# Kernel tuning notes

Hardware: AMD Instinct MI355X
Metric: run time of the kernel (lower is better)

Reference implementation:

```python
import jax, jax.numpy as jnp
import numpy as np


def conv2d_relu(x, W, b, stride=1):
    # x: NHWC, W: HWIO
    y = jax.lax.conv_general_dilated(x, W, (stride, stride), 'VALID',
                                     dimension_numbers=('NHWC', 'HWIO', 'NHWC'))
    return jax.nn.relu(y + b)


def maxpool_3x3_s2(x):
    return jax.lax.reduce_window(x, -jnp.inf, jax.lax.max,
                                 (1, 3, 3, 1), (1, 2, 2, 1), 'VALID')


def locally_connected_relu(x, W, b, k, stride=1):
    # x: [B, H, W, C]; W: [oh, ow, C*k*k, F]; b: [oh, ow, F]
    # Extract patches -> [B, oh, ow, C*k*k], then per-position GEMM.
    p = jax.lax.conv_general_dilated_patches(
        x, (k, k), (stride, stride), 'VALID',
        dimension_numbers=('NHWC', 'HWIO', 'NHWC'))
    return jax.nn.relu(jnp.einsum('bijp,ijpf->bijf', p, W) + b)


def setup_inputs() -> dict:
    key = jax.random.key(0)
    ks = jax.random.split(key, 16)
    s = 0.02  # small init so relu/sigmoid stay in a sane range
    inp = {
        'inputs': jax.random.normal(ks[0], (32, 152, 152, 3), dtype=jnp.float32),
        'W1': jax.random.normal(ks[1], (11, 11, 3, 32), dtype=jnp.float32) * s,
        'b1': jnp.zeros((32,), jnp.float32),
        'W3': jax.random.normal(ks[2], (9, 9, 32, 16), dtype=jnp.float32) * s,
        'b3': jnp.zeros((16,), jnp.float32),
        'LW4': jax.random.normal(ks[3], (54, 54, 9 * 9 * 16, 16), dtype=jnp.float32) * s,
        'Lb4': jnp.zeros((54, 54, 16), jnp.float32),
        'LW5': jax.random.normal(ks[4], (24, 24, 7 * 7 * 16, 16), dtype=jnp.float32) * s,
        'Lb5': jnp.zeros((24, 24, 16), jnp.float32),
        'LW6': jax.random.normal(ks[5], (20, 20, 5 * 5 * 16, 16), dtype=jnp.float32) * s,
        'Lb6': jnp.zeros((20, 20, 16), jnp.float32),
        'W7': jax.random.normal(ks[6], (6400, 4096), dtype=jnp.float32) * s,
        'b7': jnp.zeros((4096,), jnp.float32),
        'W8': jax.random.normal(ks[7], (4096, 1), dtype=jnp.float32) * s,
        'b8': jnp.zeros((1,), jnp.float32),
    }
    return inp


def reference(inputs, W1, b1, W3, b3, LW4, Lb4, LW5, Lb5, LW6, Lb6, W7, b7, W8, b8):
    x = conv2d_relu(inputs, W1, b1)          # [B,142,142,32]
    x = maxpool_3x3_s2(x)                    # [B,70,70,32]
    x = conv2d_relu(x, W3, b3)               # [B,62,62,16]
    x = locally_connected_relu(x, LW4, Lb4, 9, 1)   # [B,54,54,16]
    x = locally_connected_relu(x, LW5, Lb5, 7, 2)   # [B,24,24,16]
    x = locally_connected_relu(x, LW6, Lb6, 5, 1)   # [B,20,20,16]
    x = x.reshape(x.shape[0], -1)            # [B,6400]
    x = jax.nn.relu(x @ W7 + b7)             # [B,4096]  (Dropout is identity at inference)
    return jax.nn.sigmoid(x @ W8 + b8)       # [B,1]
```

## Files before the change

### kernel.cpp

```cpp
#include <hip/hip_runtime.h>
#include <math.h>

#define DEV_INLINE __device__ __forceinline__

DEV_INLINE float relu_f(float v) { return v > 0.f ? v : 0.f; }

DEV_INLINE void fma4(float4& a, float s, const float4& v) {
    a.x += s * v.x; a.y += s * v.y; a.z += s * v.z; a.w += s * v.w;
}

__global__ __launch_bounds__(256, 2) void k_conv1(
    const float* __restrict__ x, const float* __restrict__ W,
    const float* __restrict__ b, float* __restrict__ y)
{
    __shared__ float sw[11 * 11 * 3 * 32];
    __shared__ float sx[26 * 42 * 3];
    const int n   = blockIdx.z;
    const int oh0 = blockIdx.y * 16;
    const int ow0 = blockIdx.x * 32;
    const int tid = threadIdx.x;

    for (int i = tid; i < 11616; i += 256) sw[i] = W[i];

    const float* xn = x + (size_t)n * 152 * 152 * 3;
    for (int i = tid; i < 26 * 42 * 3; i += 256) {
        int c = i % 3; int t = i / 3; int col = t % 42; int row = t / 42;
        int r  = oh0 + row; if (r > 151) r = 151;
        int cc = ow0 + col; if (cc > 151) cc = 151;
        sx[i] = xn[(r * 152 + cc) * 3 + c];
    }
    __syncthreads();

    const int ty = tid >> 4, tx = tid & 15;
    float acc[2][32];
#pragma unroll
    for (int p = 0; p < 2; ++p)
#pragma unroll
        for (int j = 0; j < 32; ++j) acc[p][j] = 0.f;

    for (int kh = 0; kh < 11; ++kh) {
        for (int kw = 0; kw < 11; ++kw) {
#pragma unroll
            for (int ic = 0; ic < 3; ++ic) {
                float x0 = sx[((ty + kh) * 42 + (tx + kw)) * 3 + ic];
                float x1 = sx[((ty + kh) * 42 + (tx + 16 + kw)) * 3 + ic];
                const float4* wp4 = (const float4*)&sw[((kh * 11 + kw) * 3 + ic) * 32];
#pragma unroll
                for (int j4 = 0; j4 < 8; ++j4) {
                    float4 w = wp4[j4];
                    acc[0][j4 * 4 + 0] += x0 * w.x;
                    acc[0][j4 * 4 + 1] += x0 * w.y;
                    acc[0][j4 * 4 + 2] += x0 * w.z;
                    acc[0][j4 * 4 + 3] += x0 * w.w;
                    acc[1][j4 * 4 + 0] += x1 * w.x;
                    acc[1][j4 * 4 + 1] += x1 * w.y;
                    acc[1][j4 * 4 + 2] += x1 * w.z;
                    acc[1][j4 * 4 + 3] += x1 * w.w;
                }
            }
        }
    }

#pragma unroll
    for (int p = 0; p < 2; ++p) {
        int oh = oh0 + ty, ow = ow0 + tx + p * 16;
        if (oh < 142 && ow < 142) {
            float* yp = y + (((size_t)n * 142 + oh) * 142 + ow) * 32;
#pragma unroll
            for (int j = 0; j < 32; ++j) yp[j] = relu_f(acc[p][j] + b[j]);
        }
    }
}

__global__ void k_pool(const float* __restrict__ x, float* __restrict__ y)
{
    int idx = blockIdx.x * 256 + threadIdx.x;
    if (idx >= 32 * 70 * 70 * 8) return;
    int c4 = idx & 7; int t = idx >> 3;
    int pw = t % 70; t /= 70; int ph = t % 70; int n = t / 70;
    const float* xp = x + (((size_t)n * 142 + ph * 2) * 142 + pw * 2) * 32 + c4 * 4;
    float4 m = make_float4(-1e30f, -1e30f, -1e30f, -1e30f);
#pragma unroll
    for (int r = 0; r < 3; ++r) {
#pragma unroll
        for (int cc = 0; cc < 3; ++cc) {
            float4 v = *(const float4*)(xp + ((size_t)r * 142 + cc) * 32);
            m.x = fmaxf(m.x, v.x); m.y = fmaxf(m.y, v.y);
            m.z = fmaxf(m.z, v.z); m.w = fmaxf(m.w, v.w);
        }
    }
    *(float4*)(y + (size_t)idx * 4) = m;
}

__global__ __launch_bounds__(128, 2) void k_conv3(
    const float* __restrict__ x, const float* __restrict__ W,
    const float* __restrict__ bias, float* __restrict__ y)
{
    __shared__ float sw[81 * 8 * 16];
    __shared__ float sx[16 * 40 * 8];
    const int n   = blockIdx.z;
    const int oh0 = blockIdx.y * 8;
    const int ow0 = blockIdx.x * 32;
    const int tid = threadIdx.x;
    const int ty = tid >> 4, tx = tid & 15;
    const float* xn = x + (size_t)n * 70 * 70 * 32;

    float acc[2][16];
#pragma unroll
    for (int p = 0; p < 2; ++p)
#pragma unroll
        for (int j = 0; j < 16; ++j) acc[p][j] = 0.f;

    for (int icc = 0; icc < 4; ++icc) {
        const int ic0 = icc * 8;
        __syncthreads();
        for (int i = tid; i < 10368; i += 128) {
            int oc = i & 15; int t = i >> 4; int ic = t & 7; int q = t >> 3;
            sw[i] = W[(q * 32 + ic0 + ic) * 16 + oc];
        }
        for (int i = tid; i < 5120; i += 128) {
            int ic = i & 7; int t = i >> 3; int col = t % 40; int row = t / 40;
            int r  = oh0 + row; if (r > 69) r = 69;
            int cc = ow0 + col; if (cc > 69) cc = 69;
            sx[i] = xn[(r * 70 + cc) * 32 + ic0 + ic];
        }
        __syncthreads();

        for (int kh = 0; kh < 9; ++kh) {
            for (int kw = 0; kw < 9; ++kw) {
                const int q = kh * 9 + kw;
#pragma unroll
                for (int ic = 0; ic < 8; ++ic) {
                    float x0 = sx[((ty + kh) * 40 + tx + kw) * 8 + ic];
                    float x1 = sx[((ty + kh) * 40 + tx + 16 + kw) * 8 + ic];
                    const float4* wp4 = (const float4*)&sw[(q * 8 + ic) * 16];
#pragma unroll
                    for (int j4 = 0; j4 < 4; ++j4) {
                        float4 w = wp4[j4];
                        acc[0][j4 * 4 + 0] += x0 * w.x;
                        acc[0][j4 * 4 + 1] += x0 * w.y;
                        acc[0][j4 * 4 + 2] += x0 * w.z;
                        acc[0][j4 * 4 + 3] += x0 * w.w;
                        acc[1][j4 * 4 + 0] += x1 * w.x;
                        acc[1][j4 * 4 + 1] += x1 * w.y;
                        acc[1][j4 * 4 + 2] += x1 * w.z;
                        acc[1][j4 * 4 + 3] += x1 * w.w;
                    }
                }
            }
        }
    }

#pragma unroll
    for (int p = 0; p < 2; ++p) {
        int oh = oh0 + ty, ow = ow0 + tx + p * 16;
        if (oh < 62 && ow < 62) {
            float* yp = y + (((size_t)n * 62 + oh) * 62 + ow) * 16;
#pragma unroll
            for (int j = 0; j < 16; ++j) yp[j] = relu_f(acc[p][j] + bias[j]);
        }
    }
}

template <int K, int S, int XD, int OD>
__global__ __launch_bounds__(64) void k_lc(
    const float* __restrict__ x, const float* __restrict__ W,
    const float* __restrict__ bias, float* __restrict__ y)
{
    constexpr int K2 = K * K;
    constexpr int P  = 16 * K2;
    __shared__ int soff[K2];
    const int i = blockIdx.y, j = blockIdx.x;
    const int tid = threadIdx.x;
    for (int t = tid; t < K2; t += 64) {
        int kh = t / K, kw = t % K;
        soff[t] = ((i * S + kh) * XD + (j * S + kw)) * 16;
    }
    __syncthreads();

    const int fq = tid & 3, b0 = tid >> 2;
    const float* xb0 = x + (size_t)b0 * XD * XD * 16;
    const float* xb1 = xb0 + (size_t)16 * XD * XD * 16;
    const float* wp  = W + ((size_t)(i * OD + j) * P) * 16 + fq * 4;

    float4 a0 = make_float4(0.f, 0.f, 0.f, 0.f);
    float4 a1 = make_float4(0.f, 0.f, 0.f, 0.f);

    for (int q = 0; q < K2; ++q) {
        const int ro = soff[q];
#pragma unroll
        for (int c4 = 0; c4 < 4; ++c4) {
            const float4 xv0 = *(const float4*)(xb0 + ro + c4 * 4);
            const float4 xv1 = *(const float4*)(xb1 + ro + c4 * 4);
            const float4 w0 = *(const float4*)(wp + ((c4 * 4 + 0) * K2 + q) * 16);
            const float4 w1 = *(const float4*)(wp + ((c4 * 4 + 1) * K2 + q) * 16);
            const float4 w2 = *(const float4*)(wp + ((c4 * 4 + 2) * K2 + q) * 16);
            const float4 w3 = *(const float4*)(wp + ((c4 * 4 + 3) * K2 + q) * 16);
            fma4(a0, xv0.x, w0); fma4(a0, xv0.y, w1); fma4(a0, xv0.z, w2); fma4(a0, xv0.w, w3);
            fma4(a1, xv1.x, w0); fma4(a1, xv1.y, w1); fma4(a1, xv1.z, w2); fma4(a1, xv1.w, w3);
        }
    }

    const float4 bv = *(const float4*)(bias + ((size_t)i * OD + j) * 16 + fq * 4);
    a0.x = relu_f(a0.x + bv.x); a0.y = relu_f(a0.y + bv.y);
    a0.z = relu_f(a0.z + bv.z); a0.w = relu_f(a0.w + bv.w);
    a1.x = relu_f(a1.x + bv.x); a1.y = relu_f(a1.y + bv.y);
    a1.z = relu_f(a1.z + bv.z); a1.w = relu_f(a1.w + bv.w);
    *(float4*)(y + (((size_t)b0 * OD + i) * OD + j) * 16 + fq * 4) = a0;
    *(float4*)(y + (((size_t)(b0 + 16) * OD + i) * OD + j) * 16 + fq * 4) = a1;
}

__global__ __launch_bounds__(256) void k_fc7(
    const float* __restrict__ x, const float* __restrict__ W,
    float* __restrict__ part)
{
    const int o  = blockIdx.x * 256 + threadIdx.x;
    const int k0 = blockIdx.y * 400;
    float acc[32];
#pragma unroll
    for (int b = 0; b < 32; ++b) acc[b] = 0.f;
    const float* wp = W + (size_t)k0 * 4096 + o;
    for (int kk = 0; kk < 400; kk += 2) {
        float w0 = wp[(size_t)kk * 4096];
        float w1 = wp[(size_t)(kk + 1) * 4096];
#pragma unroll
        for (int b = 0; b < 32; ++b) {
            float2 xv = *(const float2*)(x + (size_t)b * 6400 + k0 + kk);
            acc[b] += xv.x * w0 + xv.y * w1;
        }
    }
    float* pp = part + ((size_t)blockIdx.y * 32) * 4096 + o;
#pragma unroll
    for (int b = 0; b < 32; ++b) pp[(size_t)b * 4096] = acc[b];
}

__global__ __launch_bounds__(256) void k_fc8(
    const float* __restrict__ part, const float* __restrict__ b7,
    const float* __restrict__ W8, const float* __restrict__ b8,
    float* __restrict__ out)
{
    const int b = blockIdx.x, tid = threadIdx.x;
    float s = 0.f;
    for (int o = tid; o < 4096; o += 256) {
        float v = b7[o];
#pragma unroll
        for (int kb = 0; kb < 16; ++kb) v += part[((size_t)kb * 32 + b) * 4096 + o];
        v = relu_f(v);
        s += v * W8[o];
    }
#pragma unroll
    for (int off = 32; off > 0; off >>= 1) s += __shfl_down(s, off, 64);
    __shared__ float red[4];
    if ((tid & 63) == 0) red[tid >> 6] = s;
    __syncthreads();
    if (tid == 0) {
        float t = red[0] + red[1] + red[2] + red[3] + b8[0];
        out[b] = 1.f / (1.f + expf(-t));
    }
}

extern "C" void kernel_launch(void* const* d_in, const int* in_sizes, int n_in,
                              void* d_out, int out_size, void* d_ws, size_t ws_size,
                              hipStream_t stream)
{
    (void)in_sizes; (void)n_in; (void)out_size; (void)ws_size;
    const float* x   = (const float*)d_in[0];
    const float* W1  = (const float*)d_in[1];
    const float* b1  = (const float*)d_in[2];
    const float* W3  = (const float*)d_in[3];
    const float* b3  = (const float*)d_in[4];
    const float* LW4 = (const float*)d_in[5];
    const float* Lb4 = (const float*)d_in[6];
    const float* LW5 = (const float*)d_in[7];
    const float* Lb5 = (const float*)d_in[8];
    const float* LW6 = (const float*)d_in[9];
    const float* Lb6 = (const float*)d_in[10];
    const float* W7  = (const float*)d_in[11];
    const float* b7  = (const float*)d_in[12];
    const float* W8  = (const float*)d_in[13];
    const float* b8  = (const float*)d_in[14];
    float* out = (float*)d_out;

    float* ws = (float*)d_ws;
    float* y1 = ws;
    float* y2 = ws + 20647936;
    float* y3 = ws;
    float* y4 = ws + 1968128;
    float* y5 = ws + 3461120;
    float* y6 = ws + 3756032;
    float* p7 = ws + 3960832;

    k_conv1<<<dim3(5, 9, 32), 256, 0, stream>>>(x, W1, b1, y1);
    k_pool<<<dim3(4900), 256, 0, stream>>>(y1, y2);
    k_conv3<<<dim3(2, 8, 32), 128, 0, stream>>>(y2, W3, b3, y3);
    k_lc<9, 1, 62, 54><<<dim3(54, 54), 64, 0, stream>>>(y3, LW4, Lb4, y4);
    k_lc<7, 2, 54, 24><<<dim3(24, 24), 64, 0, stream>>>(y4, LW5, Lb5, y5);
    k_lc<5, 1, 24, 20><<<dim3(20, 20), 64, 0, stream>>>(y5, LW6, Lb6, y6);
    k_fc7<<<dim3(16, 16), 256, 0, stream>>>(y6, W7, p7);
    k_fc8<<<dim3(32), 256, 0, stream>>>(p7, b7, W8, b8, out);
}
```

Baseline: 1.333 ms.

## Stage locally-connected weights through shared memory in channel groups

The locally-connected kernels now cooperatively copy each position's weights into LDS in channel-group stages, and all 32 batch threads-groups read weights from shared memory instead of each re-reading them from global memory. The block grows to 128 threads, one batch element per 4 threads, so each thread keeps a single float4 accumulator instead of two. Each stage adds two barriers, and the per-layer group size is chosen to fit LDS. The global weight loads used to be duplicated across threads, and that duplication is what this targets.

```diff
diff --git a/kernel.cpp b/kernel.cpp
--- a/kernel.cpp
+++ b/kernel.cpp
@@ -162,52 +162,55 @@
     }
 }
 
-template <int K, int S, int XD, int OD>
-__global__ __launch_bounds__(64) void k_lc(
+template <int K, int S, int XD, int OD, int GC>
+__global__ __launch_bounds__(128) void k_lc(
     const float* __restrict__ x, const float* __restrict__ W,
     const float* __restrict__ bias, float* __restrict__ y)
 {
-    constexpr int K2 = K * K;
-    constexpr int P  = 16 * K2;
-    __shared__ int soff[K2];
+    constexpr int K2     = K * K;
+    constexpr int STAGES = 16 / GC;
+    constexpr int SPAN4  = GC * K2 * 4;
+    __shared__ float sw[GC * K2 * 16];
+
     const int i = blockIdx.y, j = blockIdx.x;
     const int tid = threadIdx.x;
-    for (int t = tid; t < K2; t += 64) {
-        int kh = t / K, kw = t % K;
-        soff[t] = ((i * S + kh) * XD + (j * S + kw)) * 16;
-    }
-    __syncthreads();
-
-    const int fq = tid & 3, b0 = tid >> 2;
-    const float* xb0 = x + (size_t)b0 * XD * XD * 16;
-    const float* xb1 = xb0 + (size_t)16 * XD * XD * 16;
-    const float* wp  = W + ((size_t)(i * OD + j) * P) * 16 + fq * 4;
-
-    float4 a0 = make_float4(0.f, 0.f, 0.f, 0.f);
-    float4 a1 = make_float4(0.f, 0.f, 0.f, 0.f);
-
-    for (int q = 0; q < K2; ++q) {
-        const int ro = soff[q];
-#pragma unroll
-        for (int c4 = 0; c4 < 4; ++c4) {
-            const float4 xv0 = *(const float4*)(xb0 + ro + c4 * 4);
-            const float4 xv1 = *(const float4*)(xb1 + ro + c4 * 4);
-            const float4 w0 = *(const float4*)(wp + ((c4 * 4 + 0) * K2 + q) * 16);
-            const float4 w1 = *(const float4*)(wp + ((c4 * 4 + 1) * K2 + q) * 16);
-            const float4 w2 = *(const float4*)(wp + ((c4 * 4 + 2) * K2 + q) * 16);
-            const float4 w3 = *(const float4*)(wp + ((c4 * 4 + 3) * K2 + q) * 16);
-            fma4(a0, xv0.x, w0); fma4(a0, xv0.y, w1); fma4(a0, xv0.z, w2); fma4(a0, xv0.w, w3);
-            fma4(a1, xv1.x, w0); fma4(a1, xv1.y, w1); fma4(a1, xv1.z, w2); fma4(a1, xv1.w, w3);
-        }
-    }
-
-    const float4 bv = *(const float4*)(bias + ((size_t)i * OD + j) * 16 + fq * 4);
-    a0.x = relu_f(a0.x + bv.x); a0.y = relu_f(a0.y + bv.y);
-    a0.z = relu_f(a0.z + bv.z); a0.w = relu_f(a0.w + bv.w);
-    a1.x = relu_f(a1.x + bv.x); a1.y = relu_f(a1.y + bv.y);
-    a1.z = relu_f(a1.z + bv.z); a1.w = relu_f(a1.w + bv.w);
-    *(float4*)(y + (((size_t)b0 * OD + i) * OD + j) * 16 + fq * 4) = a0;
-    *(float4*)(y + (((size_t)(b0 + 16) * OD + i) * OD + j) * 16 + fq * 4) = a1;
+    const int f4 = tid & 3, b = tid >> 2;
+
+    const float* xb = x + ((size_t)b * XD * XD + (size_t)(i * S) * XD + (j * S)) * 16;
+    const float4* wsrc_base = (const float4*)(W + (size_t)(i * OD + j) * (K2 * 16) * 16);
+
+    float4 acc = make_float4(0.f, 0.f, 0.f, 0.f);
+
+    for (int st = 0; st < STAGES; ++st) {
+        const int c0 = st * GC;
+        __syncthreads();
+        const float4* wsrc = wsrc_base + (size_t)c0 * K2 * 4;
+        for (int t = tid; t < SPAN4; t += 128)
+            ((float4*)sw)[t] = wsrc[t];
+        __syncthreads();
+
+        for (int kh = 0; kh < K; ++kh) {
+            const float* xrow = xb + (size_t)(kh * XD) * 16 + c0;
+            for (int kw = 0; kw < K; ++kw) {
+                const int q = kh * K + kw;
+                const float* xr = xrow + kw * 16;
+#pragma unroll
+                for (int cq = 0; cq < GC / 4; ++cq) {
+                    const float4 xv = *(const float4*)(xr + cq * 4);
+                    const int cb = cq * 4;
+                    fma4(acc, xv.x, *(const float4*)&sw[((cb + 0) * K2 + q) * 16 + f4 * 4]);
+                    fma4(acc, xv.y, *(const float4*)&sw[((cb + 1) * K2 + q) * 16 + f4 * 4]);
+                    fma4(acc, xv.z, *(const float4*)&sw[((cb + 2) * K2 + q) * 16 + f4 * 4]);
+                    fma4(acc, xv.w, *(const float4*)&sw[((cb + 3) * K2 + q) * 16 + f4 * 4]);
+                }
+            }
+        }
+    }
+
+    const float4 bv = *(const float4*)(bias + ((size_t)i * OD + j) * 16 + f4 * 4);
+    acc.x = relu_f(acc.x + bv.x); acc.y = relu_f(acc.y + bv.y);
+    acc.z = relu_f(acc.z + bv.z); acc.w = relu_f(acc.w + bv.w);
+    *(float4*)(y + (((size_t)b * OD + i) * OD + j) * 16 + f4 * 4) = acc;
 }
 
 __global__ __launch_bounds__(256) void k_fc7(
@@ -293,9 +296,9 @@
     k_conv1<<<dim3(5, 9, 32), 256, 0, stream>>>(x, W1, b1, y1);
     k_pool<<<dim3(4900), 256, 0, stream>>>(y1, y2);
     k_conv3<<<dim3(2, 8, 32), 128, 0, stream>>>(y2, W3, b3, y3);
-    k_lc<9, 1, 62, 54><<<dim3(54, 54), 64, 0, stream>>>(y3, LW4, Lb4, y4);
-    k_lc<7, 2, 54, 24><<<dim3(24, 24), 64, 0, stream>>>(y4, LW5, Lb5, y5);
-    k_lc<5, 1, 24, 20><<<dim3(20, 20), 64, 0, stream>>>(y5, LW6, Lb6, y6);
+    k_lc<9, 1, 62, 54, 4><<<dim3(54, 54), 128, 0, stream>>>(y3, LW4, Lb4, y4);
+    k_lc<7, 2, 54, 24, 8><<<dim3(24, 24), 128, 0, stream>>>(y4, LW5, Lb5, y5);
+    k_lc<5, 1, 24, 20, 16><<<dim3(20, 20), 128, 0, stream>>>(y5, LW6, Lb6, y6);
     k_fc7<<<dim3(16, 16), 256, 0, stream>>>(y6, W7, p7);
     k_fc8<<<dim3(32), 256, 0, stream>>>(p7, b7, W8, b8, out);
 }
```

Result: faster. 1.170 ms (-12.2%).
